# Performance work log

Hardware: AMD Instinct MI355X
Metric: run time of the kernel (lower is better)

## Reference

```python
import jax, jax.numpy as jnp
import numpy as np

NEG_FILL = -1.0e9
PROB_MIN = 1e-9


def _lstm_cell(x, h, c, w_ih, w_hh, b_ih, b_hh):
    # PyTorch gate order: input, forget, cell(g), output
    gates = x @ w_ih.T + h @ w_hh.T + b_ih + b_hh
    i, f, g, o = jnp.split(gates, 4, axis=-1)
    c_new = jax.nn.sigmoid(f) * c + jax.nn.sigmoid(i) * jnp.tanh(g)
    h_new = jax.nn.sigmoid(o) * jnp.tanh(c_new)
    return h_new, c_new


def setup_inputs() -> dict:
    key = jax.random.key(0)
    B, T, D, H, W = 2048, 100, 128, 256, 256
    ks = jax.random.split(key, 16)
    s_d = 1.0 / np.sqrt(D)
    s_h = 1.0 / np.sqrt(H)
    s_w = 1.0 / np.sqrt(W)
    return {
        "targets": jax.random.normal(ks[0], (B, T, D), jnp.float32),
        "h0": jax.random.normal(ks[1], (1, B, H), jnp.float32),
        "c0": jax.random.normal(ks[2], (1, B, H), jnp.float32),
        "enc_w_ih": jax.random.normal(ks[3], (4 * H, D), jnp.float32) * s_d,
        "enc_w_hh": jax.random.normal(ks[4], (4 * H, H), jnp.float32) * s_h,
        "enc_b_ih": jax.random.normal(ks[5], (4 * H,), jnp.float32) * s_h,
        "enc_b_hh": jax.random.normal(ks[6], (4 * H,), jnp.float32) * s_h,
        "dec_w_ih": jax.random.normal(ks[7], (4 * H, D), jnp.float32) * s_d,
        "dec_w_hh": jax.random.normal(ks[8], (4 * H, H), jnp.float32) * s_h,
        "dec_b_ih": jax.random.normal(ks[9], (4 * H,), jnp.float32) * s_h,
        "dec_b_hh": jax.random.normal(ks[10], (4 * H,), jnp.float32) * s_h,
        "W1": jax.random.normal(ks[11], (W, H), jnp.float32) * s_h,
        "W2": jax.random.normal(ks[12], (W, H), jnp.float32) * s_h,
        "vt": jax.random.normal(ks[13], (W,), jnp.float32) * s_w,
    }


def reference(targets, h0, c0, enc_w_ih, enc_w_hh, enc_b_ih, enc_b_hh,
              dec_w_ih, dec_w_hh, dec_b_ih, dec_b_hh, W1, W2, vt):
    B, T, D = targets.shape
    H = enc_w_hh.shape[1]

    # ---- encoder LSTM (batch_first, zero initial state) ----
    def enc_step(carry, x_t):
        h, c = carry
        h, c = _lstm_cell(x_t, h, c, enc_w_ih, enc_w_hh, enc_b_ih, enc_b_hh)
        return (h, c), h

    z = jnp.zeros((B, H), targets.dtype)
    _, enc_h = jax.lax.scan(enc_step, (z, z), jnp.swapaxes(targets, 0, 1))
    encoder_states = jnp.swapaxes(enc_h, 0, 1)  # [B, T, H]

    blend1 = encoder_states @ W1.T  # [B, T, W]

    a1 = jnp.arange(B)
    init = (h0[0], c0[0], jnp.zeros((B, T), dtype=bool), jnp.zeros_like(targets[:, 0]))

    def dec_step(carry, _):
        h, c, selected, dec_in = carry
        h, c = _lstm_cell(dec_in, h, c, dec_w_ih, dec_w_hh, dec_b_ih, dec_b_hh)
        blend2 = h @ W2.T                                   # [B, W]
        scores = jnp.tanh(blend1 + blend2[:, None, :]) @ vt  # [B, T]
        scores = jnp.where(selected, NEG_FILL, scores)
        sel = jnp.argmax(scores, axis=-1)                    # [B]
        selected = selected.at[a1, sel].set(True)
        probs = jnp.maximum(jax.nn.softmax(scores, axis=-1), PROB_MIN)
        dec_in = targets[a1, sel]                            # [B, D]
        return (h, c, selected, dec_in), probs

    _, probs = jax.lax.scan(dec_step, init, None, length=T)
    return jnp.swapaxes(probs, 0, 1)  # [B, T, T]
```

## Files before the change

kernel.cpp:

```cpp
#include <hip/hip_runtime.h>
#include <math.h>

#define BB   2048
#define TT   100
#define DD   128
#define HH   256
#define NEGF -1.0e9f

__device__ __forceinline__ float sigmoidf_(float x){ return 1.0f/(1.0f+expf(-x)); }

__global__ __launch_bounds__(256) void k_zero_i32(int* __restrict__ p, int n){
  int i = blockIdx.x*256 + threadIdx.x;
  if(i < n) p[i] = 0;
}

__global__ __launch_bounds__(256) void k_gates_cell(
    const float* __restrict__ Xp, int ldx,
    const float* __restrict__ Hp,
    const float* __restrict__ Wih, const float* __restrict__ Whh,
    const float* __restrict__ bih, const float* __restrict__ bhh,
    const float* __restrict__ Cp,
    float* __restrict__ Hout, float* __restrict__ Cout,
    float* __restrict__ Hcopy, int hstride)
{
  __shared__ alignas(16) float smem[8704];
  float* Xs = smem;
  float* Ws = smem + 4224;
  const int tid = threadIdx.x;
  const int tx = tid & 15, ty = tid >> 4;
  const int j0 = blockIdx.x * 16;
  const int m0 = blockIdx.y * 128;

  float acc[8][4];
  #pragma unroll
  for(int i=0;i<8;i++)
    #pragma unroll
    for(int j=0;j<4;j++) acc[i][j] = 0.f;

  for(int phase=0; phase<2; phase++){
    const float* Am; int lda; const float* Wm; int ldw; int nt;
    if(phase==0){ if(!Xp) continue; Am=Xp; lda=ldx; Wm=Wih; ldw=DD; nt=4; }
    else        { if(!Hp) continue; Am=Hp; lda=HH;  Wm=Whh; ldw=HH; nt=8; }
    for(int kt=0; kt<nt; kt++){
      const int k0 = kt*32;
      #pragma unroll
      for(int it=0; it<4; it++){
        int q = it*256 + tid; int m = q>>3; int kq = (q&7)<<2;
        const float4 v = *(const float4*)(Am + (size_t)(m0+m)*lda + k0 + kq);
        Xs[(kq+0)*132+m]=v.x; Xs[(kq+1)*132+m]=v.y; Xs[(kq+2)*132+m]=v.z; Xs[(kq+3)*132+m]=v.w;
      }
      #pragma unroll
      for(int it=0; it<2; it++){
        int q = it*256 + tid; int c = q>>3; int kq = (q&7)<<2;
        int n = (c>>4)*HH + j0 + (c&15);
        const float4 v = *(const float4*)(Wm + (size_t)n*ldw + k0 + kq);
        Ws[(kq+0)*68+c]=v.x; Ws[(kq+1)*68+c]=v.y; Ws[(kq+2)*68+c]=v.z; Ws[(kq+3)*68+c]=v.w;
      }
      __syncthreads();
      #pragma unroll
      for(int kk=0; kk<32; kk++){
        const float4 a0 = *(const float4*)&Xs[kk*132 + ty*8];
        const float4 a1 = *(const float4*)&Xs[kk*132 + ty*8 + 4];
        const float4 bv = *(const float4*)&Ws[kk*68 + tx*4];
        const float a[8] = {a0.x,a0.y,a0.z,a0.w,a1.x,a1.y,a1.z,a1.w};
        const float b[4] = {bv.x,bv.y,bv.z,bv.w};
        #pragma unroll
        for(int i=0;i<8;i++)
          #pragma unroll
          for(int j=0;j<4;j++)
            acc[i][j] = fmaf(a[i], b[j], acc[i][j]);
      }
      __syncthreads();
    }
  }

  float* gsm = smem;
  #pragma unroll
  for(int i=0;i<8;i++){
    *(float4*)&gsm[(ty*8+i)*68 + tx*4] = make_float4(acc[i][0],acc[i][1],acc[i][2],acc[i][3]);
  }
  __syncthreads();

  {
    const int m   = tid >> 1;
    const int jj0 = (tid & 1) * 8;
    const int b   = m0 + m;
    #pragma unroll
    for(int i=0;i<8;i++){
      const int jj  = jj0 + i;
      const int col = j0 + jj;
      const float iv = gsm[m*68 +      jj] + bih[       col] + bhh[       col];
      const float fv = gsm[m*68 + 16 + jj] + bih[  HH + col] + bhh[  HH + col];
      const float gv = gsm[m*68 + 32 + jj] + bih[2*HH + col] + bhh[2*HH + col];
      const float ov = gsm[m*68 + 48 + jj] + bih[3*HH + col] + bhh[3*HH + col];
      const size_t idx = (size_t)b*HH + col;
      const float cp = Cp ? Cp[idx] : 0.f;
      const float cn = sigmoidf_(fv)*cp + sigmoidf_(iv)*tanhf(gv);
      const float hn = sigmoidf_(ov)*tanhf(cn);
      Cout[idx] = cn;
      Hout[idx] = hn;
      if(Hcopy) Hcopy[(size_t)b*hstride + col] = hn;
    }
  }
}

__global__ __launch_bounds__(256) void k_gemm_nt(
    const float* __restrict__ A, int lda,
    const float* __restrict__ Bm, int ldb,
    float* __restrict__ C, int ldc, int K)
{
  __shared__ alignas(16) float Xs[32*68];
  __shared__ alignas(16) float Ws[32*68];
  const int tid = threadIdx.x;
  const int tx = tid & 15, ty = tid >> 4;
  const int n0 = blockIdx.x*64, m0 = blockIdx.y*64;
  float acc[4][4];
  #pragma unroll
  for(int i=0;i<4;i++)
    #pragma unroll
    for(int j=0;j<4;j++) acc[i][j]=0.f;

  for(int k0=0; k0<K; k0+=32){
    #pragma unroll
    for(int it=0; it<2; it++){
      int q = it*256 + tid; int m = q>>3; int kq = (q&7)<<2;
      float4 v = *(const float4*)(A + (size_t)(m0+m)*lda + k0 + kq);
      Xs[(kq+0)*68+m]=v.x; Xs[(kq+1)*68+m]=v.y; Xs[(kq+2)*68+m]=v.z; Xs[(kq+3)*68+m]=v.w;
      v = *(const float4*)(Bm + (size_t)(n0+m)*ldb + k0 + kq);
      Ws[(kq+0)*68+m]=v.x; Ws[(kq+1)*68+m]=v.y; Ws[(kq+2)*68+m]=v.z; Ws[(kq+3)*68+m]=v.w;
    }
    __syncthreads();
    #pragma unroll
    for(int kk=0; kk<32; kk++){
      const float4 av = *(const float4*)&Xs[kk*68 + ty*4];
      const float4 bv = *(const float4*)&Ws[kk*68 + tx*4];
      const float a[4] = {av.x,av.y,av.z,av.w};
      const float b[4] = {bv.x,bv.y,bv.z,bv.w};
      #pragma unroll
      for(int i=0;i<4;i++)
        #pragma unroll
        for(int j=0;j<4;j++)
          acc[i][j] = fmaf(a[i], b[j], acc[i][j]);
    }
    __syncthreads();
  }
  #pragma unroll
  for(int i=0;i<4;i++){
    *(float4*)&C[(size_t)(m0+ty*4+i)*ldc + n0 + tx*4] =
        make_float4(acc[i][0],acc[i][1],acc[i][2],acc[i][3]);
  }
}

__global__ __launch_bounds__(256) void k_blend1(float* __restrict__ blend1,
                                                const float* __restrict__ W1)
{
  __shared__ alignas(16) float Af[32*260];
  __shared__ alignas(16) float Ws[32*68];
  const int tid = threadIdx.x;
  const int tx = tid & 15, ty = tid >> 4;
  const size_t r0 = (size_t)blockIdx.x * 32;

  #pragma unroll
  for(int it=0; it<8; it++){
    int q = it*256 + tid; int m = q>>6; int kq = (q&63)<<2;
    *(float4*)&Af[m*260 + kq] = *(const float4*)(blend1 + (r0+m)*256 + kq);
  }
  __syncthreads();

  for(int nc=0; nc<4; nc++){
    const int n0 = nc*64;
    float acc[2][4];
    #pragma unroll
    for(int i=0;i<2;i++)
      #pragma unroll
      for(int j=0;j<4;j++) acc[i][j]=0.f;
    for(int kt=0; kt<8; kt++){
      const int k0 = kt*32;
      __syncthreads();
      #pragma unroll
      for(int it=0; it<2; it++){
        int q = it*256 + tid; int c = q>>3; int kq = (q&7)<<2;
        const float4 v = *(const float4*)(W1 + (size_t)(n0+c)*256 + k0 + kq);
        Ws[(kq+0)*68+c]=v.x; Ws[(kq+1)*68+c]=v.y; Ws[(kq+2)*68+c]=v.z; Ws[(kq+3)*68+c]=v.w;
      }
      __syncthreads();
      #pragma unroll
      for(int kk=0; kk<32; kk++){
        const float4 bv = *(const float4*)&Ws[kk*68 + tx*4];
        const float a0 = Af[(ty*2+0)*260 + k0 + kk];
        const float a1 = Af[(ty*2+1)*260 + k0 + kk];
        acc[0][0]=fmaf(a0,bv.x,acc[0][0]); acc[0][1]=fmaf(a0,bv.y,acc[0][1]);
        acc[0][2]=fmaf(a0,bv.z,acc[0][2]); acc[0][3]=fmaf(a0,bv.w,acc[0][3]);
        acc[1][0]=fmaf(a1,bv.x,acc[1][0]); acc[1][1]=fmaf(a1,bv.y,acc[1][1]);
        acc[1][2]=fmaf(a1,bv.z,acc[1][2]); acc[1][3]=fmaf(a1,bv.w,acc[1][3]);
      }
    }
    #pragma unroll
    for(int i=0;i<2;i++){
      *(float4*)&blend1[(r0 + ty*2 + i)*256 + n0 + tx*4] =
          make_float4(acc[i][0],acc[i][1],acc[i][2],acc[i][3]);
    }
  }
}

__global__ __launch_bounds__(256) void k_scores(
    const float* __restrict__ blend1,
    const float* __restrict__ blend2,
    const float* __restrict__ vt,
    const float* __restrict__ targets,
    int*  __restrict__ selected,
    float* __restrict__ dec_in,
    float* __restrict__ out,
    int s)
{
  __shared__ float vt_s[256], b2_s[256], sc[128];
  __shared__ float M_s, S_s;
  __shared__ int sel_s;
  const int b = blockIdx.x;
  const int tid = threadIdx.x;
  const int lane = tid & 63;
  const int wave = tid >> 6;

  vt_s[tid] = vt[tid];
  b2_s[tid] = blend2[(size_t)b*256 + tid];
  __syncthreads();

  for(int it=0; it<25; it++){
    const int t = wave + it*4;
    const float* row = blend1 + ((size_t)b*TT + t)*256;
    float p = 0.f;
    #pragma unroll
    for(int r=0; r<4; r++){
      const int k = lane + r*64;
      p = fmaf(tanhf(row[k] + b2_s[k]), vt_s[k], p);
    }
    #pragma unroll
    for(int off=32; off>=1; off>>=1) p += __shfl_xor(p, off, 64);
    if(lane == 0) sc[t] = p;
  }
  __syncthreads();

  if(wave == 0){
    float m1 = selected[(size_t)b*TT + lane] ? NEGF : sc[lane];
    sc[lane] = m1;
    float bestv = m1; int besti = lane;
    float m2 = 0.f;
    const int t2 = lane + 64;
    if(t2 < TT){
      m2 = selected[(size_t)b*TT + t2] ? NEGF : sc[t2];
      sc[t2] = m2;
      if(m2 > bestv){ bestv = m2; besti = t2; }
    }
    #pragma unroll
    for(int off=32; off>=1; off>>=1){
      const float ov = __shfl_xor(bestv, off, 64);
      const int   oi = __shfl_xor(besti, off, 64);
      if(ov > bestv || (ov == bestv && oi < besti)){ bestv = ov; besti = oi; }
    }
    float e = expf(m1 - bestv);
    if(t2 < TT) e += expf(m2 - bestv);
    #pragma unroll
    for(int off=32; off>=1; off>>=1) e += __shfl_xor(e, off, 64);
    if(lane == 0){
      M_s = bestv; S_s = e; sel_s = besti;
      selected[(size_t)b*TT + besti] = 1;
    }
  }
  __syncthreads();

  const int sel = sel_s;
  if(tid < TT){
    float p = expf(sc[tid] - M_s) / S_s;
    out[(size_t)b*TT*TT + (size_t)s*TT + tid] = fmaxf(p, 1e-9f);
  }
  if(tid < DD){
    dec_in[(size_t)b*DD + tid] = targets[((size_t)b*TT + sel)*DD + tid];
  }
}

extern "C" void kernel_launch(void* const* d_in, const int* in_sizes, int n_in,
                              void* d_out, int out_size, void* d_ws, size_t ws_size,
                              hipStream_t stream)
{
  (void)in_sizes; (void)n_in; (void)out_size; (void)ws_size;
  const float* targets  = (const float*)d_in[0];
  const float* h0       = (const float*)d_in[1];
  const float* c0       = (const float*)d_in[2];
  const float* enc_w_ih = (const float*)d_in[3];
  const float* enc_w_hh = (const float*)d_in[4];
  const float* enc_b_ih = (const float*)d_in[5];
  const float* enc_b_hh = (const float*)d_in[6];
  const float* dec_w_ih = (const float*)d_in[7];
  const float* dec_w_hh = (const float*)d_in[8];
  const float* dec_b_ih = (const float*)d_in[9];
  const float* dec_b_hh = (const float*)d_in[10];
  const float* W1       = (const float*)d_in[11];
  const float* W2       = (const float*)d_in[12];
  const float* vt       = (const float*)d_in[13];
  float* out = (float*)d_out;

  float* ws      = (float*)d_ws;
  float* blend1  = ws;
  float* hA      = blend1 + (size_t)BB*TT*256;
  float* hB      = hA + (size_t)BB*HH;
  float* cA      = hB + (size_t)BB*HH;
  float* cB      = cA + (size_t)BB*HH;
  float* blend2  = cB + (size_t)BB*HH;
  float* dec_in  = blend2 + (size_t)BB*HH;
  int*   selected= (int*)(dec_in + (size_t)BB*DD);

  k_zero_i32<<<(BB*TT + 255)/256, 256, 0, stream>>>(selected, BB*TT);

  for(int t=0; t<TT; t++){
    const float* Hp = (t==0) ? nullptr : ((t&1) ? hA : hB);
    const float* Cp = (t==0) ? nullptr : ((t&1) ? cA : cB);
    float* Ho = (t&1) ? hB : hA;
    float* Co = (t&1) ? cB : cA;
    k_gates_cell<<<dim3(16,16), 256, 0, stream>>>(
        targets + (size_t)t*DD, TT*DD,
        Hp, enc_w_ih, enc_w_hh, enc_b_ih, enc_b_hh, Cp,
        Ho, Co, blend1 + (size_t)t*256, TT*256);
  }

  k_blend1<<<BB*TT/32, 256, 0, stream>>>(blend1, W1);

  for(int s=0; s<TT; s++){
    const float* Hp = (s==0) ? h0 : ((s&1) ? hA : hB);
    const float* Cp = (s==0) ? c0 : ((s&1) ? cA : cB);
    float* Ho = (s&1) ? hB : hA;
    float* Co = (s&1) ? cB : cA;
    const float* Xp = (s==0) ? nullptr : dec_in;
    k_gates_cell<<<dim3(16,16), 256, 0, stream>>>(
        Xp, DD, Hp, dec_w_ih, dec_w_hh, dec_b_ih, dec_b_hh, Cp,
        Ho, Co, nullptr, 0);
    k_gemm_nt<<<dim3(4,32), 256, 0, stream>>>(Ho, HH, W2, HH, blend2, HH, HH);
    k_scores<<<BB, 256, 0, stream>>>(blend1, blend2, vt, targets, selected,
                                     dec_in, out, s);
  }
}
```

Before: 14.78 ms.

## Retile LSTM gate kernel with interleaved gate columns and fast tanh in scores

```diff
diff --git a/kernel.cpp b/kernel.cpp
--- a/kernel.cpp
+++ b/kernel.cpp
@@ -9,12 +9,18 @@
 
 __device__ __forceinline__ float sigmoidf_(float x){ return 1.0f/(1.0f+expf(-x)); }
 
+__device__ __forceinline__ float tanh_fast(float x){
+  x = fminf(15.f, fmaxf(-15.f, x));
+  const float e = __expf(x + x);
+  return (e - 1.f) * __builtin_amdgcn_rcpf(e + 1.f);
+}
+
 __global__ __launch_bounds__(256) void k_zero_i32(int* __restrict__ p, int n){
   int i = blockIdx.x*256 + threadIdx.x;
   if(i < n) p[i] = 0;
 }
 
-__global__ __launch_bounds__(256) void k_gates_cell(
+__global__ __launch_bounds__(128) void k_gates_cell(
     const float* __restrict__ Xp, int ldx,
     const float* __restrict__ Hp,
     const float* __restrict__ Wih, const float* __restrict__ Whh,
@@ -23,19 +29,19 @@
     float* __restrict__ Hout, float* __restrict__ Cout,
     float* __restrict__ Hcopy, int hstride)
 {
-  __shared__ alignas(16) float smem[8704];
-  float* Xs = smem;
-  float* Ws = smem + 4224;
+  __shared__ alignas(16) float Xs[32*68];
+  __shared__ alignas(16) float Ws[32*68];
   const int tid = threadIdx.x;
-  const int tx = tid & 15, ty = tid >> 4;
+  const int tx = tid & 15;
+  const int ty = tid >> 4;
   const int j0 = blockIdx.x * 16;
-  const int m0 = blockIdx.y * 128;
+  const int m0 = blockIdx.y * 64;
 
   float acc[8][4];
   #pragma unroll
   for(int i=0;i<8;i++)
     #pragma unroll
-    for(int j=0;j<4;j++) acc[i][j] = 0.f;
+    for(int s=0;s<4;s++) acc[i][s] = 0.f;
 
   for(int phase=0; phase<2; phase++){
     const float* Am; int lda; const float* Wm; int ldw; int nt;
@@ -45,62 +51,54 @@
       const int k0 = kt*32;
       #pragma unroll
       for(int it=0; it<4; it++){
-        int q = it*256 + tid; int m = q>>3; int kq = (q&7)<<2;
+        int q = it*128 + tid; int m = q>>3; int kq = (q&7)<<2;
         const float4 v = *(const float4*)(Am + (size_t)(m0+m)*lda + k0 + kq);
-        Xs[(kq+0)*132+m]=v.x; Xs[(kq+1)*132+m]=v.y; Xs[(kq+2)*132+m]=v.z; Xs[(kq+3)*132+m]=v.w;
-      }
-      #pragma unroll
-      for(int it=0; it<2; it++){
-        int q = it*256 + tid; int c = q>>3; int kq = (q&7)<<2;
-        int n = (c>>4)*HH + j0 + (c&15);
+        Xs[(kq+0)*68+m]=v.x; Xs[(kq+1)*68+m]=v.y; Xs[(kq+2)*68+m]=v.z; Xs[(kq+3)*68+m]=v.w;
+      }
+      #pragma unroll
+      for(int it=0; it<4; it++){
+        int q = it*128 + tid; int c = q>>3; int kq = (q&7)<<2;
+        int n = (c&3)*HH + j0 + (c>>2);
         const float4 v = *(const float4*)(Wm + (size_t)n*ldw + k0 + kq);
         Ws[(kq+0)*68+c]=v.x; Ws[(kq+1)*68+c]=v.y; Ws[(kq+2)*68+c]=v.z; Ws[(kq+3)*68+c]=v.w;
       }
       __syncthreads();
       #pragma unroll
       for(int kk=0; kk<32; kk++){
-        const float4 a0 = *(const float4*)&Xs[kk*132 + ty*8];
-        const float4 a1 = *(const float4*)&Xs[kk*132 + ty*8 + 4];
+        const float4 a0 = *(const float4*)&Xs[kk*68 + ty*8];
+        const float4 a1 = *(const float4*)&Xs[kk*68 + ty*8 + 4];
         const float4 bv = *(const float4*)&Ws[kk*68 + tx*4];
         const float a[8] = {a0.x,a0.y,a0.z,a0.w,a1.x,a1.y,a1.z,a1.w};
-        const float b[4] = {bv.x,bv.y,bv.z,bv.w};
+        const float g[4] = {bv.x,bv.y,bv.z,bv.w};
         #pragma unroll
         for(int i=0;i<8;i++)
           #pragma unroll
-          for(int j=0;j<4;j++)
-            acc[i][j] = fmaf(a[i], b[j], acc[i][j]);
+          for(int s=0;s<4;s++)
+            acc[i][s] = fmaf(a[i], g[s], acc[i][s]);
       }
       __syncthreads();
     }
   }
 
-  float* gsm = smem;
+  const int col = j0 + tx;
+  const float bi0 = bih[       col] + bhh[       col];
+  const float bf0 = bih[  HH + col] + bhh[  HH + col];
+  const float bg0 = bih[2*HH + col] + bhh[2*HH + col];
+  const float bo0 = bih[3*HH + col] + bhh[3*HH + col];
   #pragma unroll
   for(int i=0;i<8;i++){
-    *(float4*)&gsm[(ty*8+i)*68 + tx*4] = make_float4(acc[i][0],acc[i][1],acc[i][2],acc[i][3]);
-  }
-  __syncthreads();
-
-  {
-    const int m   = tid >> 1;
-    const int jj0 = (tid & 1) * 8;
-    const int b   = m0 + m;
-    #pragma unroll
-    for(int i=0;i<8;i++){
-      const int jj  = jj0 + i;
-      const int col = j0 + jj;
-      const float iv = gsm[m*68 +      jj] + bih[       col] + bhh[       col];
-      const float fv = gsm[m*68 + 16 + jj] + bih[  HH + col] + bhh[  HH + col];
-      const float gv = gsm[m*68 + 32 + jj] + bih[2*HH + col] + bhh[2*HH + col];
-      const float ov = gsm[m*68 + 48 + jj] + bih[3*HH + col] + bhh[3*HH + col];
-      const size_t idx = (size_t)b*HH + col;
-      const float cp = Cp ? Cp[idx] : 0.f;
-      const float cn = sigmoidf_(fv)*cp + sigmoidf_(iv)*tanhf(gv);
-      const float hn = sigmoidf_(ov)*tanhf(cn);
-      Cout[idx] = cn;
-      Hout[idx] = hn;
-      if(Hcopy) Hcopy[(size_t)b*hstride + col] = hn;
-    }
+    const int b = m0 + ty*8 + i;
+    const size_t idx = (size_t)b*HH + col;
+    const float iv = acc[i][0] + bi0;
+    const float fv = acc[i][1] + bf0;
+    const float gv = acc[i][2] + bg0;
+    const float ov = acc[i][3] + bo0;
+    const float cp = Cp ? Cp[idx] : 0.f;
+    const float cn = sigmoidf_(fv)*cp + sigmoidf_(iv)*tanhf(gv);
+    const float hn = sigmoidf_(ov)*tanhf(cn);
+    Cout[idx] = cn;
+    Hout[idx] = hn;
+    if(Hcopy) Hcopy[(size_t)b*hstride + col] = hn;
   }
 }
 
@@ -225,15 +223,17 @@
   b2_s[tid] = blend2[(size_t)b*256 + tid];
   __syncthreads();
 
+  const float4 bb = *(const float4*)&b2_s[lane*4];
+  const float4 vv = *(const float4*)&vt_s[lane*4];
+
   for(int it=0; it<25; it++){
     const int t = wave + it*4;
-    const float* row = blend1 + ((size_t)b*TT + t)*256;
-    float p = 0.f;
-    #pragma unroll
-    for(int r=0; r<4; r++){
-      const int k = lane + r*64;
-      p = fmaf(tanhf(row[k] + b2_s[k]), vt_s[k], p);
-    }
+    const float4 x = *(const float4*)(blend1 + ((size_t)b*TT + t)*256 + lane*4);
+    float p;
+    p = tanh_fast(x.x + bb.x) * vv.x;
+    p = fmaf(tanh_fast(x.y + bb.y), vv.y, p);
+    p = fmaf(tanh_fast(x.z + bb.z), vv.z, p);
+    p = fmaf(tanh_fast(x.w + bb.w), vv.w, p);
     #pragma unroll
     for(int off=32; off>=1; off>>=1) p += __shfl_xor(p, off, 64);
     if(lane == 0) sc[t] = p;
@@ -257,8 +257,8 @@
       const int   oi = __shfl_xor(besti, off, 64);
       if(ov > bestv || (ov == bestv && oi < besti)){ bestv = ov; besti = oi; }
     }
-    float e = expf(m1 - bestv);
-    if(t2 < TT) e += expf(m2 - bestv);
+    float e = __expf(m1 - bestv);
+    if(t2 < TT) e += __expf(m2 - bestv);
     #pragma unroll
     for(int off=32; off>=1; off>>=1) e += __shfl_xor(e, off, 64);
     if(lane == 0){
@@ -270,7 +270,7 @@
 
   const int sel = sel_s;
   if(tid < TT){
-    float p = expf(sc[tid] - M_s) / S_s;
+    float p = __expf(sc[tid] - M_s) / S_s;
     out[(size_t)b*TT*TT + (size_t)s*TT + tid] = fmaxf(p, 1e-9f);
   }
   if(tid < DD){
@@ -316,7 +316,7 @@
     const float* Cp = (t==0) ? nullptr : ((t&1) ? cA : cB);
     float* Ho = (t&1) ? hB : hA;
     float* Co = (t&1) ? cB : cA;
-    k_gates_cell<<<dim3(16,16), 256, 0, stream>>>(
+    k_gates_cell<<<dim3(16,32), 128, 0, stream>>>(
         targets + (size_t)t*DD, TT*DD,
         Hp, enc_w_ih, enc_w_hh, enc_b_ih, enc_b_hh, Cp,
         Ho, Co, blend1 + (size_t)t*256, TT*256);
@@ -330,7 +330,7 @@
     float* Ho = (s&1) ? hB : hA;
     float* Co = (s&1) ? cB : cA;
     const float* Xp = (s==0) ? nullptr : dec_in;
-    k_gates_cell<<<dim3(16,16), 256, 0, stream>>>(
+    k_gates_cell<<<dim3(16,32), 128, 0, stream>>>(
         Xp, DD, Hp, dec_w_ih, dec_w_hh, dec_b_ih, dec_b_hh, Cp,
         Ho, Co, nullptr, 0);
     k_gemm_nt<<<dim3(4,32), 256, 0, stream>>>(Ho, HH, W2, HH, blend2, HH, HH);
```

Result: faster. 14.28 ms (-3.4%).
